# Kernel tuning notes

Measured on AMD Instinct MI355X. Metric: run time of the kernel, lower is better.

The kernel has to match this reference:

```python
import jax, jax.numpy as jnp
import numpy as np

OUTPUT_DIM = 2000
INPUT_DIM = 8192
N_COLS = 2000  # must equal OUTPUT_DIM so bias broadcasts over last dim as in the torch code
SPARSITY = 0.9
BLOCK = 4


def _apply_block_sparsity(weight, block=BLOCK, sparsity=SPARSITY, seed=1234):
    # Zero out 4x4 blocks with probability `sparsity`, mirroring apply_block_sparsity.
    rng = np.random.RandomState(seed)
    rb = (weight.shape[0] + block - 1) // block
    cb = (weight.shape[1] + block - 1) // block
    keep = (rng.rand(rb, cb) <= (1.0 - sparsity)).astype(np.float32)
    mask = np.kron(keep, np.ones((block, block), dtype=np.float32))
    return weight * mask[: weight.shape[0], : weight.shape[1]]


def setup_inputs() -> dict:
    key = jax.random.key(0)
    k_w, k_b, k_x = jax.random.split(key, 3)
    weight = np.asarray(jax.random.normal(k_w, (OUTPUT_DIM, INPUT_DIM), dtype=jnp.float32))
    weight = jnp.asarray(_apply_block_sparsity(weight))
    bias = jax.random.normal(k_b, (OUTPUT_DIM,), dtype=jnp.float32)
    x = jax.random.normal(k_x, (INPUT_DIM, N_COLS), dtype=jnp.float32)
    return {"weight": weight, "bias": bias, "x": x}


def reference(weight, bias, x):
    # [OUT, IN] @ [IN, N] -> [OUT, N]; bias [OUT] broadcasts over last dim (N == OUT here),
    # exactly matching torch.matmul(weight, x) + bias.
    return jnp.matmul(weight, x) + bias
```

## Files before the change

kernel.cpp:

```cpp
#include <hip/hip_runtime.h>

#define K_DIM 8192
#define M_REAL 2000
#define N_REAL 2000
#define M_PAD 2048
#define N_PAD 2048

#define BM 256
#define BN 256
#define BK 32
#define SPLITK 4
#define KSLAB (K_DIM / SPLITK)
#define NSTEP (KSLAB / BK)

#define NB_W 1024
#define NB_X 2048
#define NB_I 256

typedef __bf16 bf16x8 __attribute__((ext_vector_type(8)));
typedef float f32x4 __attribute__((ext_vector_type(4)));
typedef float fvec4 __attribute__((ext_vector_type(4)));

#define RAW_BARRIER()  asm volatile("s_barrier" ::: "memory")
#define WAIT_VM8()     asm volatile("s_waitcnt vmcnt(8)" ::: "memory")
#define WAIT_VM4()     asm volatile("s_waitcnt vmcnt(4)" ::: "memory")
#define WAIT_VM0()     asm volatile("s_waitcnt vmcnt(0)" ::: "memory")

__device__ __forceinline__ unsigned short f2bf(float f) {
    union { float f; unsigned u; } v; v.f = f;
    unsigned r = v.u + 0x7FFFu + ((v.u >> 16) & 1u);
    return (unsigned short)(r >> 16);
}

__device__ __forceinline__ unsigned pk2(float a, float b) {
    return (unsigned)f2bf(a) | ((unsigned)f2bf(b) << 16);
}

__device__ __forceinline__ void async16(const void* g, void* l) {
    __builtin_amdgcn_global_load_lds((__attribute__((address_space(1))) void*)(g),
                                     (__attribute__((address_space(3))) void*)(l),
                                     16, 0, 0);
}

__global__ __launch_bounds__(256) void prep_kernel(const float* __restrict__ W,
                                                   const float* __restrict__ X,
                                                   const float* __restrict__ bias,
                                                   unsigned short* __restrict__ Wb,
                                                   unsigned short* __restrict__ XT,
                                                   float* __restrict__ out) {
    __shared__ unsigned short T[64][130];
    int bid = blockIdx.x;
    if (bid < NB_W) {
        unsigned tid = bid * 256u + threadIdx.x;
#pragma unroll
        for (unsigned i = 0; i < 8; ++i) {
            unsigned e = (i * (1024u * 256u) + tid) * 8u;
            uint4 o = make_uint4(0u, 0u, 0u, 0u);
            if (e < (unsigned)(M_REAL * K_DIM)) {
                fvec4 f0 = __builtin_nontemporal_load((const fvec4*)(W + e));
                fvec4 f1 = __builtin_nontemporal_load((const fvec4*)(W + e + 4));
                o.x = pk2(f0.x, f0.y);
                o.y = pk2(f0.z, f0.w);
                o.z = pk2(f1.x, f1.y);
                o.w = pk2(f1.z, f1.w);
            }
            *(uint4*)(Wb + e) = o;
        }
    } else if (bid < NB_W + NB_X) {
        int b = bid - NB_W;
        int k0 = (b & 63) << 7;
        int n0 = (b >> 6) << 6;
        int t = threadIdx.x;
        int c = t & 15;
        int r = t >> 4;
        int nl = c << 2;
        int n = n0 + nl;
        bool valid = (n < N_REAL);
#pragma unroll
        for (int p = 0; p < 4; ++p) {
            int kl = (r << 1) + (p << 5);
            fvec4 v0 = {0.f, 0.f, 0.f, 0.f};
            fvec4 v1 = {0.f, 0.f, 0.f, 0.f};
            if (valid) {
                v0 = __builtin_nontemporal_load((const fvec4*)(X + (k0 + kl) * N_REAL + n));
                v1 = __builtin_nontemporal_load((const fvec4*)(X + (k0 + kl + 1) * N_REAL + n));
            }
            *(unsigned*)&T[nl + 0][kl] = pk2(v0.x, v1.x);
            *(unsigned*)&T[nl + 1][kl] = pk2(v0.y, v1.y);
            *(unsigned*)&T[nl + 2][kl] = pk2(v0.z, v1.z);
            *(unsigned*)&T[nl + 3][kl] = pk2(v0.w, v1.w);
        }
        __syncthreads();
#pragma unroll
        for (int it = 0; it < 4; ++it) {
            int nl2 = r + (it << 4);
            int kl2 = c << 3;
            const unsigned* tp = (const unsigned*)&T[nl2][kl2];
            uint4 o;
            o.x = tp[0]; o.y = tp[1]; o.z = tp[2]; o.w = tp[3];
            *(uint4*)(XT + (((n0 + nl2) << 13) + k0 + kl2)) = o;
        }
    } else {
        const int total = M_REAL * (N_REAL / 4);
        for (int i = (bid - NB_W - NB_X) * 256 + (int)threadIdx.x; i < total; i += NB_I * 256) {
            int m = i / (N_REAL / 4);
            int n4 = i - m * (N_REAL / 4);
            float4 bv = *(const float4*)(bias + (n4 << 2));
            *(float4*)(out + m * N_REAL + (n4 << 2)) = bv;
        }
    }
}

__global__ __launch_bounds__(512, 2) void gemm_kernel(const unsigned short* __restrict__ Wb,
                                                      const unsigned short* __restrict__ XT,
                                                      float* __restrict__ out) {
    __shared__ __align__(16) unsigned short As[4][BM * BK];
    __shared__ __align__(16) unsigned short Bs[4][BN * BK];

    int f = blockIdx.x;
    int xcd = f & 7;
    int local = f >> 3;
    int bz = local & 3;
    int bx = (xcd & 3) * 2 + ((local >> 2) & 1);
    int by = (xcd >> 2) * 4 + (local >> 3);

    int t = threadIdx.x;
    int w = t >> 6;
    int l = t & 63;
    int wm = (w >> 2) * 128;
    int wn = (w & 3) * 64;
    int lane16 = l & 15;
    int quad = l >> 4;
    int m0 = by * BM;
    int n0 = bx * BN;
    int ks = bz * KSLAB;

    f32x4 acc[8][4] = {};

    int rlin = t >> 2;
    int ck = (t & 3) ^ ((rlin >> 1) & 3);
    const unsigned short* gA0 = Wb + (long long)(m0 + rlin) * K_DIM + ks + ck * 8;
    const unsigned short* gA1 = gA0 + 128LL * K_DIM;
    const unsigned short* gB0 = XT + (long long)(n0 + rlin) * K_DIM + ks + ck * 8;
    const unsigned short* gB1 = gB0 + 128LL * K_DIM;

    char* smA = (char*)&As[0][0];
    char* smB = (char*)&Bs[0][0];
    int wslot = w * 1024;

#define STAGE_A(OFF) do { \
        async16(gA0, smA + (OFF) + wslot); \
        async16(gA1, smA + (OFF) + 8192 + wslot); \
        gA0 += BK; gA1 += BK; } while (0)
#define STAGE_B(OFF) do { \
        async16(gB0, smB + (OFF) + wslot); \
        async16(gB1, smB + (OFF) + 8192 + wslot); \
        gB0 += BK; gB1 += BK; } while (0)

    int swz = ((quad ^ ((lane16 >> 1) & 3)) << 4);
    int arow = (wm + lane16) * 64 + swz;
    int brow = (wn + lane16) * 64 + swz;

    STAGE_A(0);     STAGE_B(0);
    STAGE_A(16384); STAGE_B(16384);
    STAGE_A(32768); STAGE_B(32768);
    WAIT_VM8();
    RAW_BARRIER();

    int cur = 0;
    int stg = 49152;

    bf16x8 a0, a1, a2, a3, b0, b1, b2, b3;

    for (int s = 0; s < NSTEP; ++s) {
        const char* ab = smA + cur + arow;
        const char* bb = smB + cur + brow;
        a0 = *(const bf16x8*)(ab);
        a1 = *(const bf16x8*)(ab + 1024);
        a2 = *(const bf16x8*)(ab + 2048);
        a3 = *(const bf16x8*)(ab + 3072);
        b0 = *(const bf16x8*)(bb);
        b1 = *(const bf16x8*)(bb + 1024);
        b2 = *(const bf16x8*)(bb + 2048);
        b3 = *(const bf16x8*)(bb + 3072);

        if (s < NSTEP - 3) {
            STAGE_A(stg);
            STAGE_B(stg);
        }

        __builtin_amdgcn_s_setprio(1);
        acc[0][0] = __builtin_amdgcn_mfma_f32_16x16x32_bf16(a0, b0, acc[0][0], 0, 0, 0);
        acc[0][1] = __builtin_amdgcn_mfma_f32_16x16x32_bf16(a0, b1, acc[0][1], 0, 0, 0);
        acc[0][2] = __builtin_amdgcn_mfma_f32_16x16x32_bf16(a0, b2, acc[0][2], 0, 0, 0);
        acc[0][3] = __builtin_amdgcn_mfma_f32_16x16x32_bf16(a0, b3, acc[0][3], 0, 0, 0);
        acc[1][0] = __builtin_amdgcn_mfma_f32_16x16x32_bf16(a1, b0, acc[1][0], 0, 0, 0);
        acc[1][1] = __builtin_amdgcn_mfma_f32_16x16x32_bf16(a1, b1, acc[1][1], 0, 0, 0);
        acc[1][2] = __builtin_amdgcn_mfma_f32_16x16x32_bf16(a1, b2, acc[1][2], 0, 0, 0);
        acc[1][3] = __builtin_amdgcn_mfma_f32_16x16x32_bf16(a1, b3, acc[1][3], 0, 0, 0);
        acc[2][0] = __builtin_amdgcn_mfma_f32_16x16x32_bf16(a2, b0, acc[2][0], 0, 0, 0);
        acc[2][1] = __builtin_amdgcn_mfma_f32_16x16x32_bf16(a2, b1, acc[2][1], 0, 0, 0);
        acc[2][2] = __builtin_amdgcn_mfma_f32_16x16x32_bf16(a2, b2, acc[2][2], 0, 0, 0);
        acc[2][3] = __builtin_amdgcn_mfma_f32_16x16x32_bf16(a2, b3, acc[2][3], 0, 0, 0);
        acc[3][0] = __builtin_amdgcn_mfma_f32_16x16x32_bf16(a3, b0, acc[3][0], 0, 0, 0);
        acc[3][1] = __builtin_amdgcn_mfma_f32_16x16x32_bf16(a3, b1, acc[3][1], 0, 0, 0);
        acc[3][2] = __builtin_amdgcn_mfma_f32_16x16x32_bf16(a3, b2, acc[3][2], 0, 0, 0);
        acc[3][3] = __builtin_amdgcn_mfma_f32_16x16x32_bf16(a3, b3, acc[3][3], 0, 0, 0);
        __builtin_amdgcn_s_setprio(0);

        a0 = *(const bf16x8*)(ab + 4096);
        a1 = *(const bf16x8*)(ab + 5120);
        a2 = *(const bf16x8*)(ab + 6144);
        a3 = *(const bf16x8*)(ab + 7168);

        __builtin_amdgcn_s_setprio(1);
        acc[4][0] = __builtin_amdgcn_mfma_f32_16x16x32_bf16(a0, b0, acc[4][0], 0, 0, 0);
        acc[4][1] = __builtin_amdgcn_mfma_f32_16x16x32_bf16(a0, b1, acc[4][1], 0, 0, 0);
        acc[4][2] = __builtin_amdgcn_mfma_f32_16x16x32_bf16(a0, b2, acc[4][2], 0, 0, 0);
        acc[4][3] = __builtin_amdgcn_mfma_f32_16x16x32_bf16(a0, b3, acc[4][3], 0, 0, 0);
        acc[5][0] = __builtin_amdgcn_mfma_f32_16x16x32_bf16(a1, b0, acc[5][0], 0, 0, 0);
        acc[5][1] = __builtin_amdgcn_mfma_f32_16x16x32_bf16(a1, b1, acc[5][1], 0, 0, 0);
        acc[5][2] = __builtin_amdgcn_mfma_f32_16x16x32_bf16(a1, b2, acc[5][2], 0, 0, 0);
        acc[5][3] = __builtin_amdgcn_mfma_f32_16x16x32_bf16(a1, b3, acc[5][3], 0, 0, 0);
        acc[6][0] = __builtin_amdgcn_mfma_f32_16x16x32_bf16(a2, b0, acc[6][0], 0, 0, 0);
        acc[6][1] = __builtin_amdgcn_mfma_f32_16x16x32_bf16(a2, b1, acc[6][1], 0, 0, 0);
        acc[6][2] = __builtin_amdgcn_mfma_f32_16x16x32_bf16(a2, b2, acc[6][2], 0, 0, 0);
        acc[6][3] = __builtin_amdgcn_mfma_f32_16x16x32_bf16(a2, b3, acc[6][3], 0, 0, 0);
        acc[7][0] = __builtin_amdgcn_mfma_f32_16x16x32_bf16(a3, b0, acc[7][0], 0, 0, 0);
        acc[7][1] = __builtin_amdgcn_mfma_f32_16x16x32_bf16(a3, b1, acc[7][1], 0, 0, 0);
        acc[7][2] = __builtin_amdgcn_mfma_f32_16x16x32_bf16(a3, b2, acc[7][2], 0, 0, 0);
        acc[7][3] = __builtin_amdgcn_mfma_f32_16x16x32_bf16(a3, b3, acc[7][3], 0, 0, 0);
        __builtin_amdgcn_s_setprio(0);

        if (s < NSTEP - 3) {
            WAIT_VM8();
        } else if (s == NSTEP - 3) {
            WAIT_VM4();
        } else if (s == NSTEP - 2) {
            WAIT_VM0();
        }
        if (s < NSTEP - 1)
            RAW_BARRIER();

        cur = (cur + 16384) & 65535;
        stg = (stg + 16384) & 65535;
    }
#undef STAGE_A
#undef STAGE_B

#pragma unroll
    for (int j = 0; j < 4; ++j) {
        int n = n0 + wn + j * 16 + lane16;
        if (n >= N_REAL) continue;
#pragma unroll
        for (int i = 0; i < 8; ++i) {
            int mbase = m0 + wm + i * 16 + quad * 4;
#pragma unroll
            for (int r = 0; r < 4; ++r) {
                int m = mbase + r;
                if (m < M_REAL)
                    atomicAdd(&out[(long long)m * N_REAL + n], acc[i][j][r]);
            }
        }
    }
}

extern "C" void kernel_launch(void* const* d_in, const int* in_sizes, int n_in,
                              void* d_out, int out_size, void* d_ws, size_t ws_size,
                              hipStream_t stream) {
    const float* W    = (const float*)d_in[0];
    const float* bias = (const float*)d_in[1];
    const float* X    = (const float*)d_in[2];
    float* out = (float*)d_out;

    unsigned short* Wb = (unsigned short*)d_ws;
    unsigned short* XT = Wb + (long long)M_PAD * K_DIM;

    prep_kernel<<<NB_W + NB_X + NB_I, 256, 0, stream>>>(W, X, bias, Wb, XT, out);

    gemm_kernel<<<(N_PAD / BN) * (M_PAD / BM) * SPLITK, 512, 0, stream>>>(Wb, XT, out);
}
```

Measured before the change: 259.9 us.

## Shrink GEMM tiles to 128x128 with simple double-buffered LDS pipeline

Halves the block tile to 128x128 with 256 threads and 4 waves per block, giving four times as many blocks (1024 instead of 256) to fill the GPU's compute units. The hand-tuned 4-stage async pipeline with explicit vmcnt waits and raw barriers is replaced by a 2-stage double buffer synchronized with __syncthreads, and the s_setprio hints are removed. This trades lower per-block data reuse and more global/LDS traffic and atomics for better occupancy and load balance. Correctness of the double buffer depends on __syncthreads also draining the async global-to-LDS loads.

```diff
diff --git a/kernel.cpp b/kernel.cpp
--- a/kernel.cpp
+++ b/kernel.cpp
@@ -6,8 +6,8 @@
 #define M_PAD 2048
 #define N_PAD 2048
 
-#define BM 256
-#define BN 256
+#define BM 128
+#define BN 128
 #define BK 32
 #define SPLITK 4
 #define KSLAB (K_DIM / SPLITK)
@@ -20,11 +20,6 @@
 typedef __bf16 bf16x8 __attribute__((ext_vector_type(8)));
 typedef float f32x4 __attribute__((ext_vector_type(4)));
 typedef float fvec4 __attribute__((ext_vector_type(4)));
-
-#define RAW_BARRIER()  asm volatile("s_barrier" ::: "memory")
-#define WAIT_VM8()     asm volatile("s_waitcnt vmcnt(8)" ::: "memory")
-#define WAIT_VM4()     asm volatile("s_waitcnt vmcnt(4)" ::: "memory")
-#define WAIT_VM0()     asm volatile("s_waitcnt vmcnt(0)" ::: "memory")
 
 __device__ __forceinline__ unsigned short f2bf(float f) {
     union { float f; unsigned u; } v; v.f = f;
@@ -111,85 +106,71 @@
     }
 }
 
-__global__ __launch_bounds__(512, 2) void gemm_kernel(const unsigned short* __restrict__ Wb,
+__global__ __launch_bounds__(256, 4) void gemm_kernel(const unsigned short* __restrict__ Wb,
                                                       const unsigned short* __restrict__ XT,
                                                       float* __restrict__ out) {
-    __shared__ __align__(16) unsigned short As[4][BM * BK];
-    __shared__ __align__(16) unsigned short Bs[4][BN * BK];
+    __shared__ __align__(16) char smA[2 * 8192];
+    __shared__ __align__(16) char smB[2 * 8192];
 
     int f = blockIdx.x;
     int xcd = f & 7;
     int local = f >> 3;
     int bz = local & 3;
-    int bx = (xcd & 3) * 2 + ((local >> 2) & 1);
-    int by = (xcd >> 2) * 4 + (local >> 3);
+    int lt = local >> 2;
+    int bx = (xcd & 3) * 4 + (lt & 3);
+    int by = (xcd >> 2) * 8 + (lt >> 2);
 
     int t = threadIdx.x;
     int w = t >> 6;
     int l = t & 63;
-    int wm = (w >> 2) * 128;
-    int wn = (w & 3) * 64;
     int lane16 = l & 15;
     int quad = l >> 4;
+    int wr = w >> 1;
+    int wc = w & 1;
     int m0 = by * BM;
     int n0 = bx * BN;
     int ks = bz * KSLAB;
 
-    f32x4 acc[8][4] = {};
-
-    int rlin = t >> 2;
-    int ck = (t & 3) ^ ((rlin >> 1) & 3);
-    const unsigned short* gA0 = Wb + (long long)(m0 + rlin) * K_DIM + ks + ck * 8;
-    const unsigned short* gA1 = gA0 + 128LL * K_DIM;
-    const unsigned short* gB0 = XT + (long long)(n0 + rlin) * K_DIM + ks + ck * 8;
-    const unsigned short* gB1 = gB0 + 128LL * K_DIM;
-
-    char* smA = (char*)&As[0][0];
-    char* smB = (char*)&Bs[0][0];
-    int wslot = w * 1024;
-
-#define STAGE_A(OFF) do { \
-        async16(gA0, smA + (OFF) + wslot); \
-        async16(gA1, smA + (OFF) + 8192 + wslot); \
-        gA0 += BK; gA1 += BK; } while (0)
-#define STAGE_B(OFF) do { \
-        async16(gB0, smB + (OFF) + wslot); \
-        async16(gB1, smB + (OFF) + 8192 + wslot); \
-        gB0 += BK; gB1 += BK; } while (0)
+    f32x4 acc[4][4] = {};
+
+    int rowS = w * 32 + (l >> 2);
+    int lc   = (l & 3) ^ ((l >> 3) & 3);
+    const unsigned short* gA0 = Wb + (long long)(m0 + rowS) * K_DIM + ks + lc * 8;
+    const unsigned short* gA1 = gA0 + 16LL * K_DIM;
+    const unsigned short* gB0 = XT + (long long)(n0 + rowS) * K_DIM + ks + lc * 8;
+    const unsigned short* gB1 = gB0 + 16LL * K_DIM;
+
+#define STAGE(BUF, KOFF) do { \
+        int bo_ = (BUF) * 8192 + w * 2048; \
+        async16(gA0 + (KOFF), smA + bo_); \
+        async16(gA1 + (KOFF), smA + bo_ + 1024); \
+        async16(gB0 + (KOFF), smB + bo_); \
+        async16(gB1 + (KOFF), smB + bo_ + 1024); \
+    } while (0)
 
     int swz = ((quad ^ ((lane16 >> 1) & 3)) << 4);
-    int arow = (wm + lane16) * 64 + swz;
-    int brow = (wn + lane16) * 64 + swz;
-
-    STAGE_A(0);     STAGE_B(0);
-    STAGE_A(16384); STAGE_B(16384);
-    STAGE_A(32768); STAGE_B(32768);
-    WAIT_VM8();
-    RAW_BARRIER();
-
-    int cur = 0;
-    int stg = 49152;
-
-    bf16x8 a0, a1, a2, a3, b0, b1, b2, b3;
+    int arow = (wr * 64 + lane16) * 64 + swz;
+    int brow = (wc * 64 + lane16) * 64 + swz;
+
+    STAGE(0, 0);
+    __syncthreads();
 
     for (int s = 0; s < NSTEP; ++s) {
-        const char* ab = smA + cur + arow;
-        const char* bb = smB + cur + brow;
-        a0 = *(const bf16x8*)(ab);
-        a1 = *(const bf16x8*)(ab + 1024);
-        a2 = *(const bf16x8*)(ab + 2048);
-        a3 = *(const bf16x8*)(ab + 3072);
-        b0 = *(const bf16x8*)(bb);
-        b1 = *(const bf16x8*)(bb + 1024);
-        b2 = *(const bf16x8*)(bb + 2048);
-        b3 = *(const bf16x8*)(bb + 3072);
-
-        if (s < NSTEP - 3) {
-            STAGE_A(stg);
-            STAGE_B(stg);
-        }
-
-        __builtin_amdgcn_s_setprio(1);
+        if (s + 1 < NSTEP)
+            STAGE((s + 1) & 1, (s + 1) * BK);
+
+        int bo = (s & 1) * 8192;
+        const char* Ab = smA + bo + arow;
+        const char* Bb = smB + bo + brow;
+        bf16x8 a0 = *(const bf16x8*)(Ab);
+        bf16x8 a1 = *(const bf16x8*)(Ab + 1024);
+        bf16x8 a2 = *(const bf16x8*)(Ab + 2048);
+        bf16x8 a3 = *(const bf16x8*)(Ab + 3072);
+        bf16x8 b0 = *(const bf16x8*)(Bb);
+        bf16x8 b1 = *(const bf16x8*)(Bb + 1024);
+        bf16x8 b2 = *(const bf16x8*)(Bb + 2048);
+        bf16x8 b3 = *(const bf16x8*)(Bb + 3072);
+
         acc[0][0] = __builtin_amdgcn_mfma_f32_16x16x32_bf16(a0, b0, acc[0][0], 0, 0, 0);
         acc[0][1] = __builtin_amdgcn_mfma_f32_16x16x32_bf16(a0, b1, acc[0][1], 0, 0, 0);
         acc[0][2] = __builtin_amdgcn_mfma_f32_16x16x32_bf16(a0, b2, acc[0][2], 0, 0, 0);
@@ -206,55 +187,19 @@
         acc[3][1] = __builtin_amdgcn_mfma_f32_16x16x32_bf16(a3, b1, acc[3][1], 0, 0, 0);
         acc[3][2] = __builtin_amdgcn_mfma_f32_16x16x32_bf16(a3, b2, acc[3][2], 0, 0, 0);
         acc[3][3] = __builtin_amdgcn_mfma_f32_16x16x32_bf16(a3, b3, acc[3][3], 0, 0, 0);
-        __builtin_amdgcn_s_setprio(0);
-
-        a0 = *(const bf16x8*)(ab + 4096);
-        a1 = *(const bf16x8*)(ab + 5120);
-        a2 = *(const bf16x8*)(ab + 6144);
-        a3 = *(const bf16x8*)(ab + 7168);
-
-        __builtin_amdgcn_s_setprio(1);
-        acc[4][0] = __builtin_amdgcn_mfma_f32_16x16x32_bf16(a0, b0, acc[4][0], 0, 0, 0);
-        acc[4][1] = __builtin_amdgcn_mfma_f32_16x16x32_bf16(a0, b1, acc[4][1], 0, 0, 0);
-        acc[4][2] = __builtin_amdgcn_mfma_f32_16x16x32_bf16(a0, b2, acc[4][2], 0, 0, 0);
-        acc[4][3] = __builtin_amdgcn_mfma_f32_16x16x32_bf16(a0, b3, acc[4][3], 0, 0, 0);
-        acc[5][0] = __builtin_amdgcn_mfma_f32_16x16x32_bf16(a1, b0, acc[5][0], 0, 0, 0);
-        acc[5][1] = __builtin_amdgcn_mfma_f32_16x16x32_bf16(a1, b1, acc[5][1], 0, 0, 0);
-        acc[5][2] = __builtin_amdgcn_mfma_f32_16x16x32_bf16(a1, b2, acc[5][2], 0, 0, 0);
-        acc[5][3] = __builtin_amdgcn_mfma_f32_16x16x32_bf16(a1, b3, acc[5][3], 0, 0, 0);
-        acc[6][0] = __builtin_amdgcn_mfma_f32_16x16x32_bf16(a2, b0, acc[6][0], 0, 0, 0);
-        acc[6][1] = __builtin_amdgcn_mfma_f32_16x16x32_bf16(a2, b1, acc[6][1], 0, 0, 0);
-        acc[6][2] = __builtin_amdgcn_mfma_f32_16x16x32_bf16(a2, b2, acc[6][2], 0, 0, 0);
-        acc[6][3] = __builtin_amdgcn_mfma_f32_16x16x32_bf16(a2, b3, acc[6][3], 0, 0, 0);
-        acc[7][0] = __builtin_amdgcn_mfma_f32_16x16x32_bf16(a3, b0, acc[7][0], 0, 0, 0);
-        acc[7][1] = __builtin_amdgcn_mfma_f32_16x16x32_bf16(a3, b1, acc[7][1], 0, 0, 0);
-        acc[7][2] = __builtin_amdgcn_mfma_f32_16x16x32_bf16(a3, b2, acc[7][2], 0, 0, 0);
-        acc[7][3] = __builtin_amdgcn_mfma_f32_16x16x32_bf16(a3, b3, acc[7][3], 0, 0, 0);
-        __builtin_amdgcn_s_setprio(0);
-
-        if (s < NSTEP - 3) {
-            WAIT_VM8();
-        } else if (s == NSTEP - 3) {
-            WAIT_VM4();
-        } else if (s == NSTEP - 2) {
-            WAIT_VM0();
-        }
-        if (s < NSTEP - 1)
-            RAW_BARRIER();
-
-        cur = (cur + 16384) & 65535;
-        stg = (stg + 16384) & 65535;
+
+        if (s + 1 < NSTEP)
+            __syncthreads();
     }
-#undef STAGE_A
-#undef STAGE_B
+#undef STAGE
 
 #pragma unroll
     for (int j = 0; j < 4; ++j) {
-        int n = n0 + wn + j * 16 + lane16;
+        int n = n0 + wc * 64 + j * 16 + lane16;
         if (n >= N_REAL) continue;
 #pragma unroll
-        for (int i = 0; i < 8; ++i) {
-            int mbase = m0 + wm + i * 16 + quad * 4;
+        for (int i = 0; i < 4; ++i) {
+            int mbase = m0 + wr * 64 + i * 16 + quad * 4;
 #pragma unroll
             for (int r = 0; r < 4; ++r) {
                 int m = mbase + r;
@@ -278,5 +223,5 @@
 
     prep_kernel<<<NB_W + NB_X + NB_I, 256, 0, stream>>>(W, X, bias, Wb, XT, out);
 
-    gemm_kernel<<<(N_PAD / BN) * (M_PAD / BM) * SPLITK, 512, 0, stream>>>(Wb, XT, out);
-}
+    gemm_kernel<<<(N_PAD / BN) * (M_PAD / BM) * SPLITK, 256, 0, stream>>>(Wb, XT, out);
+}
```

After: 259.0 us. Within noise of the previous version (-0.3%).
